# Optimization experiments

Hardware: AMD Instinct MI355X
Metric: run time of the kernel (lower is better)

The kernel has to match this reference:

```python
import jax, jax.numpy as jnp
import numpy as np

N = 50000
D_IN = 128
D_OUT = 128
EPS = 1e-5


def setup_inputs() -> dict:
    key = jax.random.key(0)
    ks = jax.random.split(key, 10)
    x = jax.random.normal(ks[0], (N, D_IN), dtype=jnp.float32)
    edge_index = jax.random.randint(ks[1], (2, 800000), 0, N, dtype=jnp.int64)
    s_in = 1.0 / np.sqrt(D_IN)
    s_out = 1.0 / np.sqrt(D_OUT)
    return {
        "x": x,
        "edge_index": edge_index,
        # SAGEConv 1: lin_l (on aggregated neighbors, with bias), lin_r (root, no bias)
        "w1_l": jax.random.uniform(ks[2], (D_OUT, D_IN), jnp.float32, -s_in, s_in),
        "b1_l": jnp.zeros((D_OUT,), jnp.float32),
        "w1_r": jax.random.uniform(ks[3], (D_OUT, D_IN), jnp.float32, -s_in, s_in),
        # SAGEConv 2
        "w2_l": jax.random.uniform(ks[4], (D_OUT, D_OUT), jnp.float32, -s_out, s_out),
        "b2_l": jnp.zeros((D_OUT,), jnp.float32),
        "w2_r": jax.random.uniform(ks[5], (D_OUT, D_OUT), jnp.float32, -s_out, s_out),
        # BatchNorm affine params
        "bn_gamma": jnp.ones((D_OUT,), jnp.float32),
        "bn_beta": jnp.zeros((D_OUT,), jnp.float32),
    }


def _sage_conv(x, src, dst, w_l, b_l, w_r):
    # mean aggregation of source-node features into target nodes
    msg = x[src]                                              # [E, D]
    agg = jax.ops.segment_sum(msg, dst, num_segments=N)       # [N, D]
    cnt = jax.ops.segment_sum(jnp.ones((src.shape[0],), x.dtype), dst, num_segments=N)
    mean = agg / jnp.maximum(cnt, 1.0)[:, None]
    return mean @ w_l.T + b_l + x @ w_r.T


def _batch_norm(x, gamma, beta):
    mu = jnp.mean(x, axis=0)
    var = jnp.mean(jnp.square(x - mu), axis=0)  # biased, as in torch BN training
    return (x - mu) * jax.lax.rsqrt(var + EPS) * gamma + beta


def reference(x, edge_index, w1_l, b1_l, w1_r, w2_l, b2_l, w2_r, bn_gamma, bn_beta):
    src, dst = edge_index[0], edge_index[1]
    h = _sage_conv(x, src, dst, w1_l, b1_l, w1_r)
    h = _batch_norm(h, bn_gamma, bn_beta)
    h = jax.nn.relu(h)
    out = _sage_conv(h, src, dst, w2_l, b2_l, w2_r)
    return out
```

## Files before the change

### kernel.cpp

```cpp
#include <hip/hip_runtime.h>

#define D 128
#define EPS 1e-5f
#define FB_EPB 8

typedef unsigned int uint;
typedef __attribute__((ext_vector_type(4))) float f32x4;
typedef __attribute__((ext_vector_type(8))) short s16x8;

__device__ __forceinline__ uint pack_bf16(float a, float b)
{
    uint ua = __float_as_uint(a);
    uint ub = __float_as_uint(b);
    ua += 0x7FFFu + ((ua >> 16) & 1u);
    ub += 0x7FFFu + ((ub >> 16) & 1u);
    return (ua >> 16) | (ub & 0xFFFF0000u);
}
__device__ __forceinline__ float bf_lo(uint v) { return __uint_as_float(v << 16); }
__device__ __forceinline__ float bf_hi(uint v) { return __uint_as_float(v & 0xFFFF0000u); }

__global__ void prep_kernel(const float* __restrict__ x, uint* __restrict__ xb, int ncvt,
                            const float* __restrict__ w1l, const float* __restrict__ w1r,
                            const float* __restrict__ w2l, const float* __restrict__ w2r,
                            uint* __restrict__ wb1, uint* __restrict__ wb2)
{
    int idx = blockIdx.x * 256 + threadIdx.x;
    if (idx < ncvt) {
        float4 v = ((const float4*)x)[idx];
        uint2 o;
        o.x = pack_bf16(v.x, v.y);
        o.y = pack_bf16(v.z, v.w);
        ((uint2*)xb)[idx] = o;
    } else if (idx < ncvt + 8192) {
        int r = idx - ncvt;
        int layer = r >> 12;
        int rem = r & 4095;
        int lane = rem & 63;
        int knt = rem >> 6;
        int kstep = knt >> 3, nt = knt & 7;
        int nn = nt * 16 + (lane & 15);
        int kbase = kstep * 32 + (lane >> 4) * 8;
        const float* wl = layer ? w2l : w1l;
        const float* wr = layer ? w2r : w1r;
        uint* wb = layer ? wb2 : wb1;
        float v[8];
#pragma unroll
        for (int j = 0; j < 8; j++) {
            int k = kbase + j;
            v[j] = (k < D) ? wl[nn * D + k] : wr[nn * D + (k - D)];
        }
        uint4 o;
        o.x = pack_bf16(v[0], v[1]);
        o.y = pack_bf16(v[2], v[3]);
        o.z = pack_bf16(v[4], v[5]);
        o.w = pack_bf16(v[6], v[7]);
        ((uint4*)wb)[(kstep * 8 + nt) * 64 + lane] = o;
    } else if (idx < ncvt + 8192 + 32) {
        ((uint2*)xb)[ncvt + (idx - ncvt - 8192)] = make_uint2(0, 0);
    }
}

__global__ __launch_bounds__(512) void bcount_kernel(const int* __restrict__ dst,
                                                     int* __restrict__ bcnt,
                                                     int E, int nblk, int nbuck)
{
    __shared__ int cnt[128];
    int t = threadIdx.x;
    if (t < 128) cnt[t] = 0;
    __syncthreads();
    int e0 = blockIdx.x * (512 * FB_EPB);
#pragma unroll
    for (int k = 0; k < FB_EPB; k++) {
        int e = e0 + k * 512 + t;
        if (e < E) atomicAdd(&cnt[dst[e] >> 9], 1);
    }
    __syncthreads();
    if (t < nbuck) bcnt[t * nblk + blockIdx.x] = cnt[t];
}

__global__ __launch_bounds__(1024) void bscan_kernel(int* __restrict__ bcnt, int M)
{
    __shared__ int sums[1024];
    int t = threadIdx.x;
    int chunk = (M + 1023) / 1024;
    int b0 = t * chunk;
    int b1 = min(b0 + chunk, M);
    int v[32];
    int s = 0;
    for (int i = b0; i < b1; i++) { v[i - b0] = bcnt[i]; s += v[i - b0]; }
    sums[t] = s;
    __syncthreads();
    for (int off = 1; off < 1024; off <<= 1) {
        int u = (t >= off) ? sums[t - off] : 0;
        __syncthreads();
        sums[t] += u;
        __syncthreads();
    }
    int run = sums[t] - s;
    for (int i = b0; i < b1; i++) { bcnt[i] = run; run += v[i - b0]; }
    if (t == 1023) bcnt[M] = sums[1023];
}

__global__ __launch_bounds__(512) void bscatter_kernel(const int* __restrict__ src,
                                                       const int* __restrict__ dst,
                                                       const int* __restrict__ bcnt,
                                                       uint2* __restrict__ ebuf,
                                                       int E, int nblk, int nbuck)
{
    __shared__ int cnt[128], base[128];
    int t = threadIdx.x;
    if (t < 128) cnt[t] = 0;
    __syncthreads();
    int e0 = blockIdx.x * (512 * FB_EPB);
    int s[FB_EPB], d[FB_EPB], loc[FB_EPB];
#pragma unroll
    for (int k = 0; k < FB_EPB; k++) {
        int e = e0 + k * 512 + t;
        if (e < E) {
            s[k] = src[e];
            d[k] = dst[e];
            loc[k] = atomicAdd(&cnt[d[k] >> 9], 1);
        }
    }
    __syncthreads();
    if (t < nbuck) base[t] = bcnt[t * nblk + blockIdx.x];
    __syncthreads();
#pragma unroll
    for (int k = 0; k < FB_EPB; k++) {
        int e = e0 + k * 512 + t;
        if (e < E) {
            int b = d[k] >> 9;
            ebuf[base[b] + loc[k]] = make_uint2((uint)s[k], (uint)d[k]);
        }
    }
}

__global__ __launch_bounds__(512) void pbuild_kernel(const int* __restrict__ bcnt,
                                                     const uint2* __restrict__ ebuf,
                                                     int* __restrict__ rowptr,
                                                     int* __restrict__ col,
                                                     int n, int nblk, int nbuck, int M, int E)
{
    __shared__ int lcnt[512], lscan[512];
    int t = threadIdx.x;
    int b = blockIdx.x;
    int nb = b << 9;
    int e0 = bcnt[b * nblk];
    int e1 = (b + 1 < nbuck) ? bcnt[(b + 1) * nblk] : bcnt[M];
    lcnt[t] = 0;
    __syncthreads();
    for (int i = e0 + t; i < e1; i += 512)
        atomicAdd(&lcnt[(int)ebuf[i].y - nb], 1);
    __syncthreads();
    int s = lcnt[t];
    lscan[t] = s;
    __syncthreads();
    for (int off = 1; off < 512; off <<= 1) {
        int u = (t >= off) ? lscan[t - off] : 0;
        __syncthreads();
        lscan[t] += u;
        __syncthreads();
    }
    int start = e0 + lscan[t] - s;
    int ncnt = min(512, n - nb);
    if (t < ncnt) rowptr[nb + t] = start;
    if (b == nbuck - 1 && t == 0) rowptr[n] = E;
    lscan[t] = start;
    __syncthreads();
    for (int i = e0 + t; i < e1; i += 512) {
        uint2 ed = ebuf[i];
        int p = atomicAdd(&lscan[(int)ed.y - nb], 1);
        col[p] = (int)ed.x;
    }
}

__global__ __launch_bounds__(256) void agg_kernel(const int* __restrict__ rowptr,
                                                  const int* __restrict__ col,
                                                  const uint* __restrict__ featb,
                                                  uint* __restrict__ aggb, int n)
{
    int node = blockIdx.x * 4 + (threadIdx.x >> 6);
    if (node >= n) return;
    int lane = threadIdx.x & 63;
    int sub = lane >> 4, l16 = lane & 15;
    int r0 = rowptr[node], r1 = rowptr[node + 1];
    uint4* out4 = (uint4*)aggb;
    if (r0 == r1) {
        if (lane < 16) out4[(size_t)node * 16 + l16] = make_uint4(0, 0, 0, 0);
        return;
    }
    float acc[8] = {0.f, 0.f, 0.f, 0.f, 0.f, 0.f, 0.f, 0.f};
    const uint4* fb = (const uint4*)featb;
    int last = r1 - 1;

    for (int i = r0; i < r1; i += 16) {
        uint4 v[4];
#pragma unroll
        for (int r = 0; r < 4; r++) {
            int idx = i + r * 4 + sub;
            int cl = col[min(idx, last)];
            int c = (idx < r1) ? cl : n;
            v[r] = fb[(size_t)c * 16 + l16];
        }
#pragma unroll
        for (int r = 0; r < 4; r++) {
            uint4 u = v[r];
            acc[0] += bf_lo(u.x); acc[1] += bf_hi(u.x);
            acc[2] += bf_lo(u.y); acc[3] += bf_hi(u.y);
            acc[4] += bf_lo(u.z); acc[5] += bf_hi(u.z);
            acc[6] += bf_lo(u.w); acc[7] += bf_hi(u.w);
        }
    }
#pragma unroll
    for (int j = 0; j < 8; j++) {
        acc[j] += __shfl_down(acc[j], 32);
        acc[j] += __shfl_down(acc[j], 16);
    }
    if (lane < 16) {
        float inv = 1.0f / (float)(r1 - r0);
        uint4 o;
        o.x = pack_bf16(acc[0] * inv, acc[1] * inv);
        o.y = pack_bf16(acc[2] * inv, acc[3] * inv);
        o.z = pack_bf16(acc[4] * inv, acc[5] * inv);
        o.w = pack_bf16(acc[6] * inv, acc[7] * inv);
        out4[(size_t)node * 16 + l16] = o;
    }
}

#define TSTRIDE 132
template<bool FUSE1>
__global__ __launch_bounds__(256) void conv_kernel(
    const uint* __restrict__ p1b, const uint* __restrict__ p2b,
    const uint* __restrict__ wb, const float* __restrict__ bias,
    float* __restrict__ outf, uint* __restrict__ outb,
    float* __restrict__ pstats, int n)
{
    extern __shared__ float smem[];
    float* tile = smem;
    int w = threadIdx.x >> 6, lane = threadIdx.x & 63;
    int quad = lane >> 4, l15 = lane & 15;
    int nb = blockIdx.x * 64;

    const uint4* p1 = (const uint4*)p1b;
    const uint4* p2 = (const uint4*)p2b;
    const uint4* wv = (const uint4*)wb;

    uint4 B[8][2];
    int nt0 = w * 2;
#pragma unroll
    for (int ks = 0; ks < 8; ks++) {
#pragma unroll
        for (int t = 0; t < 2; t++)
            B[ks][t] = wv[(ks * 8 + nt0 + t) * 64 + lane];
    }

    float bv0 = bias[nt0 * 16 + l15];
    float bv1 = bias[nt0 * 16 + 16 + l15];

    for (int rt = 0; rt < 4; rt++) {
        int node = nb + rt * 16 + l15;
        int nc = min(node, n - 1);
        uint4 A[8];
#pragma unroll
        for (int ks = 0; ks < 4; ks++) A[ks] = p1[(size_t)nc * 16 + ks * 4 + quad];
#pragma unroll
        for (int ks = 0; ks < 4; ks++) A[ks + 4] = p2[(size_t)nc * 16 + ks * 4 + quad];

        f32x4 acc0 = {bv0, bv0, bv0, bv0};
        f32x4 acc1 = {bv1, bv1, bv1, bv1};
#pragma unroll
        for (int ks = 0; ks < 8; ks++) {
            s16x8 a = *(s16x8*)&A[ks];
            acc0 = __builtin_amdgcn_mfma_f32_16x16x32_bf16(a, *(s16x8*)&B[ks][0], acc0, 0, 0, 0);
            acc1 = __builtin_amdgcn_mfma_f32_16x16x32_bf16(a, *(s16x8*)&B[ks][1], acc1, 0, 0, 0);
        }
        int row0 = nb + rt * 16 + quad * 4;
        int colbase = nt0 * 16 + l15;
        if (FUSE1) {
            int rloc0 = rt * 16 + quad * 4;
#pragma unroll
            for (int reg = 0; reg < 4; reg++) {
                bool ok = (row0 + reg) < n;
                tile[(rloc0 + reg) * TSTRIDE + colbase]      = ok ? acc0[reg] : 0.f;
                tile[(rloc0 + reg) * TSTRIDE + colbase + 16] = ok ? acc1[reg] : 0.f;
            }
        } else {
#pragma unroll
            for (int reg = 0; reg < 4; reg++) {
                int row = row0 + reg;
                if (row < n) {
                    outf[(size_t)row * D + colbase] = acc0[reg];
                    outf[(size_t)row * D + colbase + 16] = acc1[reg];
                }
            }
        }
    }

    if (FUSE1) {
        __syncthreads();
        int colj = threadIdx.x & 127, half = threadIdx.x >> 7;
        float s = 0.f, ss = 0.f;
        for (int r = half * 32; r < half * 32 + 32; r++) {
            float v = tile[r * TSTRIDE + colj];
            s += v;
            ss += v * v;
        }
        float* pb = pstats + (size_t)blockIdx.x * 512 + half * 256;
        pb[colj] = s;
        pb[128 + colj] = ss;
        uint4* ob4 = (uint4*)outb;
#pragma unroll
        for (int q4 = 0; q4 < 4; q4++) {
            int idx = q4 * 256 + threadIdx.x;
            int r = idx >> 4, q = idx & 15;
            int row = nb + r;
            if (row < n) {
                float* tr = &tile[r * TSTRIDE + q * 8];
                uint4 o;
                o.x = pack_bf16(tr[0], tr[1]);
                o.y = pack_bf16(tr[2], tr[3]);
                o.z = pack_bf16(tr[4], tr[5]);
                o.w = pack_bf16(tr[6], tr[7]);
                ob4[(size_t)row * 16 + q] = o;
            }
        }
    }
}

__global__ __launch_bounds__(256) void reduce_kernel(const float* __restrict__ pstats,
                                                     float* __restrict__ stats, int nparts)
{
    int j = threadIdx.x;
    int chunk = (nparts + gridDim.x - 1) / gridDim.x;
    int p0 = blockIdx.x * chunk;
    int p1 = min(p0 + chunk, nparts);
    float s = 0.f;
    for (int p = p0; p < p1; p++) s += pstats[(size_t)p * 256 + j];
    unsafeAtomicAdd(&stats[j], s);
}

__global__ void bnfin_kernel(const float* __restrict__ stats, const float* __restrict__ gamma,
                             const float* __restrict__ beta, float* __restrict__ scsh, float n_inv)
{
    int j = threadIdx.x;
    float mean = stats[j] * n_inv;
    float var = fmaxf(stats[128 + j] * n_inv - mean * mean, 0.f);
    float sc = gamma[j] * rsqrtf(var + EPS);
    scsh[j] = sc;
    scsh[128 + j] = beta[j] - mean * sc;
}

__global__ __launch_bounds__(256) void bnapply_kernel(const uint* __restrict__ hb,
                                                      const float* __restrict__ scsh,
                                                      uint* __restrict__ hbn, int total2)
{
    __shared__ float scs[256];
    scs[threadIdx.x] = scsh[threadIdx.x];
    __syncthreads();
    int idx = blockIdx.x * 256 + threadIdx.x;
    if (blockIdx.x == 0 && threadIdx.x < 32)
        ((uint2*)hbn)[total2 + threadIdx.x] = make_uint2(0, 0);
    if (idx >= total2) return;
    int j4 = (idx & 31) * 4;
    uint2 u = ((const uint2*)hb)[idx];
    float e0 = fmaxf(bf_lo(u.x) * scs[j4 + 0] + scs[128 + j4 + 0], 0.f);
    float e1 = fmaxf(bf_hi(u.x) * scs[j4 + 1] + scs[128 + j4 + 1], 0.f);
    float e2 = fmaxf(bf_lo(u.y) * scs[j4 + 2] + scs[128 + j4 + 2], 0.f);
    float e3 = fmaxf(bf_hi(u.y) * scs[j4 + 3] + scs[128 + j4 + 3], 0.f);
    uint2 o;
    o.x = pack_bf16(e0, e1);
    o.y = pack_bf16(e2, e3);
    ((uint2*)hbn)[idx] = o;
}

extern "C" void kernel_launch(void* const* d_in, const int* in_sizes, int n_in,
                              void* d_out, int out_size, void* d_ws, size_t ws_size,
                              hipStream_t stream)
{
    const float* x     = (const float*)d_in[0];
    const int*   ei    = (const int*)d_in[1];
    const float* w1_l  = (const float*)d_in[2];
    const float* b1_l  = (const float*)d_in[3];
    const float* w1_r  = (const float*)d_in[4];
    const float* w2_l  = (const float*)d_in[5];
    const float* b2_l  = (const float*)d_in[6];
    const float* w2_r  = (const float*)d_in[7];
    const float* gamma = (const float*)d_in[8];
    const float* beta  = (const float*)d_in[9];

    int N = in_sizes[0] / D;
    int E = in_sizes[1] / 2;
    const int* src = ei;
    const int* dst = ei + E;

    int cblocks = (N + 63) / 64;
    int nbuck   = (N + 511) >> 9;
    int nblk    = (E + 4095) / 4096;
    int M       = nbuck * nblk;

    uint*  aggb   = (uint*)d_ws;
    uint*  xb     = aggb + (size_t)N * 64;
    uint*  hb     = xb + (size_t)(N + 1) * 64;
    uint*  hbn    = hb + (size_t)N * 64;
    uint*  wb1    = hbn + (size_t)(N + 1) * 64;
    uint*  wb2    = wb1 + 16384;
    uint2* ebuf   = (uint2*)(wb2 + 16384);
    float* stats  = (float*)(ebuf + E);
    float* scsh   = stats + 256;
    float* pstats = scsh + 256;
    int*   rowptr = (int*)(pstats + (size_t)cblocks * 512);
    int*   col    = rowptr + N + 1;
    int*   bcnt   = col + E;

    hipMemsetAsync(stats, 0, 256 * sizeof(float), stream);

    int ncvt = N * 32;
    int pblocks = (ncvt + 8192 + 32 + 255) / 256;
    prep_kernel<<<pblocks, 256, 0, stream>>>(x, xb, ncvt, w1_l, w1_r, w2_l, w2_r, wb1, wb2);

    int ablocks = (N + 3) / 4;

    bcount_kernel<<<nblk, 512, 0, stream>>>(dst, bcnt, E, nblk, nbuck);
    bscan_kernel<<<1, 1024, 0, stream>>>(bcnt, M);
    bscatter_kernel<<<nblk, 512, 0, stream>>>(src, dst, bcnt, ebuf, E, nblk, nbuck);
    pbuild_kernel<<<nbuck, 512, 0, stream>>>(bcnt, ebuf, rowptr, col, N, nblk, nbuck, M, E);

    agg_kernel<<<ablocks, 256, 0, stream>>>(rowptr, col, xb, aggb, N);
    conv_kernel<true><<<cblocks, 256, 64 * TSTRIDE * 4, stream>>>(
        aggb, xb, wb1, b1_l, nullptr, hb, pstats, N);

    reduce_kernel<<<32, 256, 0, stream>>>(pstats, stats, cblocks * 2);
    bnfin_kernel<<<1, 128, 0, stream>>>(stats, gamma, beta, scsh, 1.0f / (float)N);
    bnapply_kernel<<<(N * 32 + 255) / 256, 256, 0, stream>>>(hb, scsh, hbn, N * 32);

    agg_kernel<<<ablocks, 256, 0, stream>>>(rowptr, col, hbn, aggb, N);
    conv_kernel<false><<<cblocks, 256, 1024, stream>>>(
        aggb, hbn, wb2, b2_l, (float*)d_out, nullptr, nullptr, N);
}
```

Measured before the change: 252.0 us.

## Fuse whole GraphSAGE pipeline into one persistent kernel with grid barriers

Replaces the chain of about a dozen kernel launches with one persistent mega-kernel. Its phases (bf16 conversion, CSR build, aggregation, conv, BN stats, BN apply, second layer) are separated by a hierarchical atomic grid barrier. CSR construction moves from bucketed sort to degree count, scan and atomic-cursor scatter. The conv1 epilogue writes bf16 and accumulates BN stats directly, dropping the LDS tile. This removes launch and inter-kernel gaps, but limits occupancy to co-resident blocks, adds barrier spin costs, and makes the col order nondeterministic.

```diff
diff --git a/kernel.cpp b/kernel.cpp
--- a/kernel.cpp
+++ b/kernel.cpp
@@ -2,7 +2,6 @@
 
 #define D 128
 #define EPS 1e-5f
-#define FB_EPB 8
 
 typedef unsigned int uint;
 typedef __attribute__((ext_vector_type(4))) float f32x4;
@@ -19,228 +18,106 @@
 __device__ __forceinline__ float bf_lo(uint v) { return __uint_as_float(v << 16); }
 __device__ __forceinline__ float bf_hi(uint v) { return __uint_as_float(v & 0xFFFF0000u); }
 
-__global__ void prep_kernel(const float* __restrict__ x, uint* __restrict__ xb, int ncvt,
-                            const float* __restrict__ w1l, const float* __restrict__ w1r,
-                            const float* __restrict__ w2l, const float* __restrict__ w2r,
-                            uint* __restrict__ wb1, uint* __restrict__ wb2)
-{
-    int idx = blockIdx.x * 256 + threadIdx.x;
-    if (idx < ncvt) {
-        float4 v = ((const float4*)x)[idx];
-        uint2 o;
-        o.x = pack_bf16(v.x, v.y);
-        o.y = pack_bf16(v.z, v.w);
-        ((uint2*)xb)[idx] = o;
-    } else if (idx < ncvt + 8192) {
-        int r = idx - ncvt;
-        int layer = r >> 12;
-        int rem = r & 4095;
-        int lane = rem & 63;
-        int knt = rem >> 6;
-        int kstep = knt >> 3, nt = knt & 7;
-        int nn = nt * 16 + (lane & 15);
-        int kbase = kstep * 32 + (lane >> 4) * 8;
-        const float* wl = layer ? w2l : w1l;
-        const float* wr = layer ? w2r : w1r;
-        uint* wb = layer ? wb2 : wb1;
-        float v[8];
+struct MP {
+    const float *x, *w1l, *b1l, *w1r, *w2l, *b2l, *w2r, *gamma, *beta;
+    const int *src, *dst;
+    float *outf;
+    uint *xb, *aggb, *hb, *hbn, *wb1, *wb2;
+    int *rowptr, *cursor, *col, *bsum, *bar;
+    float *pstats, *stats, *scsh;
+    int n, e;
+};
+
+__device__ __forceinline__ void grid_barrier(int* bar, int G, int phase)
+{
+    __syncthreads();
+    if (threadIdx.x == 0) {
+        __threadfence();
+        int g = blockIdx.x >> 4;
+        int ngroups = (G + 15) >> 4;
+        int members = min(16, G - (g << 4));
+        int a = __hip_atomic_fetch_add(&bar[g * 32], 1, __ATOMIC_ACQ_REL,
+                                       __HIP_MEMORY_SCOPE_AGENT);
+        if (a + 1 == phase * members)
+            __hip_atomic_fetch_add(&bar[4096], 1, __ATOMIC_ACQ_REL,
+                                   __HIP_MEMORY_SCOPE_AGENT);
+        while (__hip_atomic_load(&bar[4096], __ATOMIC_ACQUIRE,
+                                 __HIP_MEMORY_SCOPE_AGENT) < phase * ngroups)
+            __builtin_amdgcn_s_sleep(2);
+        __threadfence();
+    }
+    __syncthreads();
+}
+
+__device__ __forceinline__ void agg_phase(const int* __restrict__ rowptr,
+                                          const int* __restrict__ col,
+                                          const uint* __restrict__ featb,
+                                          uint* __restrict__ aggb, int n, int G)
+{
+    int tid = threadIdx.x;
+    int wid = tid >> 6, lane = tid & 63;
+    int sub = lane >> 4, l16 = lane & 15;
+    const uint4* fb = (const uint4*)featb;
+    uint4* out4 = (uint4*)aggb;
+    int nlb = (n + 3) >> 2;
+    for (int lb = blockIdx.x; lb < nlb; lb += G) {
+        int node = lb * 4 + wid;
+        if (node >= n) continue;
+        int r0 = rowptr[node], r1 = rowptr[node + 1];
+        if (r0 == r1) {
+            if (lane < 16) out4[(size_t)node * 16 + l16] = make_uint4(0, 0, 0, 0);
+            continue;
+        }
+        float acc[8] = {0.f, 0.f, 0.f, 0.f, 0.f, 0.f, 0.f, 0.f};
+        int last = r1 - 1;
+        for (int i = r0; i < r1; i += 16) {
+            uint4 v[4];
+#pragma unroll
+            for (int r = 0; r < 4; r++) {
+                int idx = i + r * 4 + sub;
+                int cl = col[min(idx, last)];
+                int c = (idx < r1) ? cl : n;
+                v[r] = fb[(size_t)c * 16 + l16];
+            }
+#pragma unroll
+            for (int r = 0; r < 4; r++) {
+                uint4 u = v[r];
+                acc[0] += bf_lo(u.x); acc[1] += bf_hi(u.x);
+                acc[2] += bf_lo(u.y); acc[3] += bf_hi(u.y);
+                acc[4] += bf_lo(u.z); acc[5] += bf_hi(u.z);
+                acc[6] += bf_lo(u.w); acc[7] += bf_hi(u.w);
+            }
+        }
 #pragma unroll
         for (int j = 0; j < 8; j++) {
-            int k = kbase + j;
-            v[j] = (k < D) ? wl[nn * D + k] : wr[nn * D + (k - D)];
-        }
-        uint4 o;
-        o.x = pack_bf16(v[0], v[1]);
-        o.y = pack_bf16(v[2], v[3]);
-        o.z = pack_bf16(v[4], v[5]);
-        o.w = pack_bf16(v[6], v[7]);
-        ((uint4*)wb)[(kstep * 8 + nt) * 64 + lane] = o;
-    } else if (idx < ncvt + 8192 + 32) {
-        ((uint2*)xb)[ncvt + (idx - ncvt - 8192)] = make_uint2(0, 0);
-    }
-}
-
-__global__ __launch_bounds__(512) void bcount_kernel(const int* __restrict__ dst,
-                                                     int* __restrict__ bcnt,
-                                                     int E, int nblk, int nbuck)
-{
-    __shared__ int cnt[128];
-    int t = threadIdx.x;
-    if (t < 128) cnt[t] = 0;
-    __syncthreads();
-    int e0 = blockIdx.x * (512 * FB_EPB);
-#pragma unroll
-    for (int k = 0; k < FB_EPB; k++) {
-        int e = e0 + k * 512 + t;
-        if (e < E) atomicAdd(&cnt[dst[e] >> 9], 1);
-    }
-    __syncthreads();
-    if (t < nbuck) bcnt[t * nblk + blockIdx.x] = cnt[t];
-}
-
-__global__ __launch_bounds__(1024) void bscan_kernel(int* __restrict__ bcnt, int M)
-{
-    __shared__ int sums[1024];
-    int t = threadIdx.x;
-    int chunk = (M + 1023) / 1024;
-    int b0 = t * chunk;
-    int b1 = min(b0 + chunk, M);
-    int v[32];
-    int s = 0;
-    for (int i = b0; i < b1; i++) { v[i - b0] = bcnt[i]; s += v[i - b0]; }
-    sums[t] = s;
-    __syncthreads();
-    for (int off = 1; off < 1024; off <<= 1) {
-        int u = (t >= off) ? sums[t - off] : 0;
-        __syncthreads();
-        sums[t] += u;
-        __syncthreads();
-    }
-    int run = sums[t] - s;
-    for (int i = b0; i < b1; i++) { bcnt[i] = run; run += v[i - b0]; }
-    if (t == 1023) bcnt[M] = sums[1023];
-}
-
-__global__ __launch_bounds__(512) void bscatter_kernel(const int* __restrict__ src,
-                                                       const int* __restrict__ dst,
-                                                       const int* __restrict__ bcnt,
-                                                       uint2* __restrict__ ebuf,
-                                                       int E, int nblk, int nbuck)
-{
-    __shared__ int cnt[128], base[128];
-    int t = threadIdx.x;
-    if (t < 128) cnt[t] = 0;
-    __syncthreads();
-    int e0 = blockIdx.x * (512 * FB_EPB);
-    int s[FB_EPB], d[FB_EPB], loc[FB_EPB];
-#pragma unroll
-    for (int k = 0; k < FB_EPB; k++) {
-        int e = e0 + k * 512 + t;
-        if (e < E) {
-            s[k] = src[e];
-            d[k] = dst[e];
-            loc[k] = atomicAdd(&cnt[d[k] >> 9], 1);
-        }
-    }
-    __syncthreads();
-    if (t < nbuck) base[t] = bcnt[t * nblk + blockIdx.x];
-    __syncthreads();
-#pragma unroll
-    for (int k = 0; k < FB_EPB; k++) {
-        int e = e0 + k * 512 + t;
-        if (e < E) {
-            int b = d[k] >> 9;
-            ebuf[base[b] + loc[k]] = make_uint2((uint)s[k], (uint)d[k]);
-        }
-    }
-}
-
-__global__ __launch_bounds__(512) void pbuild_kernel(const int* __restrict__ bcnt,
-                                                     const uint2* __restrict__ ebuf,
-                                                     int* __restrict__ rowptr,
-                                                     int* __restrict__ col,
-                                                     int n, int nblk, int nbuck, int M, int E)
-{
-    __shared__ int lcnt[512], lscan[512];
-    int t = threadIdx.x;
-    int b = blockIdx.x;
-    int nb = b << 9;
-    int e0 = bcnt[b * nblk];
-    int e1 = (b + 1 < nbuck) ? bcnt[(b + 1) * nblk] : bcnt[M];
-    lcnt[t] = 0;
-    __syncthreads();
-    for (int i = e0 + t; i < e1; i += 512)
-        atomicAdd(&lcnt[(int)ebuf[i].y - nb], 1);
-    __syncthreads();
-    int s = lcnt[t];
-    lscan[t] = s;
-    __syncthreads();
-    for (int off = 1; off < 512; off <<= 1) {
-        int u = (t >= off) ? lscan[t - off] : 0;
-        __syncthreads();
-        lscan[t] += u;
-        __syncthreads();
-    }
-    int start = e0 + lscan[t] - s;
-    int ncnt = min(512, n - nb);
-    if (t < ncnt) rowptr[nb + t] = start;
-    if (b == nbuck - 1 && t == 0) rowptr[n] = E;
-    lscan[t] = start;
-    __syncthreads();
-    for (int i = e0 + t; i < e1; i += 512) {
-        uint2 ed = ebuf[i];
-        int p = atomicAdd(&lscan[(int)ed.y - nb], 1);
-        col[p] = (int)ed.x;
-    }
-}
-
-__global__ __launch_bounds__(256) void agg_kernel(const int* __restrict__ rowptr,
-                                                  const int* __restrict__ col,
-                                                  const uint* __restrict__ featb,
-                                                  uint* __restrict__ aggb, int n)
-{
-    int node = blockIdx.x * 4 + (threadIdx.x >> 6);
-    if (node >= n) return;
-    int lane = threadIdx.x & 63;
-    int sub = lane >> 4, l16 = lane & 15;
-    int r0 = rowptr[node], r1 = rowptr[node + 1];
-    uint4* out4 = (uint4*)aggb;
-    if (r0 == r1) {
-        if (lane < 16) out4[(size_t)node * 16 + l16] = make_uint4(0, 0, 0, 0);
-        return;
-    }
-    float acc[8] = {0.f, 0.f, 0.f, 0.f, 0.f, 0.f, 0.f, 0.f};
-    const uint4* fb = (const uint4*)featb;
-    int last = r1 - 1;
-
-    for (int i = r0; i < r1; i += 16) {
-        uint4 v[4];
-#pragma unroll
-        for (int r = 0; r < 4; r++) {
-            int idx = i + r * 4 + sub;
-            int cl = col[min(idx, last)];
-            int c = (idx < r1) ? cl : n;
-            v[r] = fb[(size_t)c * 16 + l16];
-        }
-#pragma unroll
-        for (int r = 0; r < 4; r++) {
-            uint4 u = v[r];
-            acc[0] += bf_lo(u.x); acc[1] += bf_hi(u.x);
-            acc[2] += bf_lo(u.y); acc[3] += bf_hi(u.y);
-            acc[4] += bf_lo(u.z); acc[5] += bf_hi(u.z);
-            acc[6] += bf_lo(u.w); acc[7] += bf_hi(u.w);
-        }
-    }
-#pragma unroll
-    for (int j = 0; j < 8; j++) {
-        acc[j] += __shfl_down(acc[j], 32);
-        acc[j] += __shfl_down(acc[j], 16);
-    }
-    if (lane < 16) {
-        float inv = 1.0f / (float)(r1 - r0);
-        uint4 o;
-        o.x = pack_bf16(acc[0] * inv, acc[1] * inv);
-        o.y = pack_bf16(acc[2] * inv, acc[3] * inv);
-        o.z = pack_bf16(acc[4] * inv, acc[5] * inv);
-        o.w = pack_bf16(acc[6] * inv, acc[7] * inv);
-        out4[(size_t)node * 16 + l16] = o;
-    }
-}
-
-#define TSTRIDE 132
+            acc[j] += __shfl_down(acc[j], 32);
+            acc[j] += __shfl_down(acc[j], 16);
+        }
+        if (lane < 16) {
+            float inv = 1.0f / (float)(r1 - r0);
+            uint4 o;
+            o.x = pack_bf16(acc[0] * inv, acc[1] * inv);
+            o.y = pack_bf16(acc[2] * inv, acc[3] * inv);
+            o.z = pack_bf16(acc[4] * inv, acc[5] * inv);
+            o.w = pack_bf16(acc[6] * inv, acc[7] * inv);
+            out4[(size_t)node * 16 + l16] = o;
+        }
+    }
+}
+
 template<bool FUSE1>
-__global__ __launch_bounds__(256) void conv_kernel(
-    const uint* __restrict__ p1b, const uint* __restrict__ p2b,
-    const uint* __restrict__ wb, const float* __restrict__ bias,
-    float* __restrict__ outf, uint* __restrict__ outb,
-    float* __restrict__ pstats, int n)
-{
-    extern __shared__ float smem[];
-    float* tile = smem;
-    int w = threadIdx.x >> 6, lane = threadIdx.x & 63;
+__device__ __forceinline__ void conv_phase(const uint* __restrict__ p1b,
+                                           const uint* __restrict__ p2b,
+                                           const uint* __restrict__ wb,
+                                           const float* __restrict__ bias,
+                                           float* __restrict__ outf,
+                                           uint* __restrict__ outb,
+                                           float* __restrict__ pstats,
+                                           int n, int G)
+{
+    int tid = threadIdx.x;
+    int w = tid >> 6, lane = tid & 63;
     int quad = lane >> 4, l15 = lane & 15;
-    int nb = blockIdx.x * 64;
-
     const uint4* p1 = (const uint4*)p1b;
     const uint4* p2 = (const uint4*)p2b;
     const uint4* wv = (const uint4*)wb;
@@ -253,124 +130,226 @@
         for (int t = 0; t < 2; t++)
             B[ks][t] = wv[(ks * 8 + nt0 + t) * 64 + lane];
     }
-
     float bv0 = bias[nt0 * 16 + l15];
     float bv1 = bias[nt0 * 16 + 16 + l15];
 
-    for (int rt = 0; rt < 4; rt++) {
-        int node = nb + rt * 16 + l15;
-        int nc = min(node, n - 1);
-        uint4 A[8];
-#pragma unroll
-        for (int ks = 0; ks < 4; ks++) A[ks] = p1[(size_t)nc * 16 + ks * 4 + quad];
-#pragma unroll
-        for (int ks = 0; ks < 4; ks++) A[ks + 4] = p2[(size_t)nc * 16 + ks * 4 + quad];
-
-        f32x4 acc0 = {bv0, bv0, bv0, bv0};
-        f32x4 acc1 = {bv1, bv1, bv1, bv1};
-#pragma unroll
-        for (int ks = 0; ks < 8; ks++) {
-            s16x8 a = *(s16x8*)&A[ks];
-            acc0 = __builtin_amdgcn_mfma_f32_16x16x32_bf16(a, *(s16x8*)&B[ks][0], acc0, 0, 0, 0);
-            acc1 = __builtin_amdgcn_mfma_f32_16x16x32_bf16(a, *(s16x8*)&B[ks][1], acc1, 0, 0, 0);
-        }
-        int row0 = nb + rt * 16 + quad * 4;
-        int colbase = nt0 * 16 + l15;
-        if (FUSE1) {
-            int rloc0 = rt * 16 + quad * 4;
-#pragma unroll
-            for (int reg = 0; reg < 4; reg++) {
-                bool ok = (row0 + reg) < n;
-                tile[(rloc0 + reg) * TSTRIDE + colbase]      = ok ? acc0[reg] : 0.f;
-                tile[(rloc0 + reg) * TSTRIDE + colbase + 16] = ok ? acc1[reg] : 0.f;
-            }
-        } else {
+    float s0 = 0.f, ss0 = 0.f, s1 = 0.f, ss1 = 0.f;
+    int ncb = (n + 63) >> 6;
+    for (int cb = blockIdx.x; cb < ncb; cb += G) {
+        int nb = cb * 64;
+        for (int rt = 0; rt < 4; rt++) {
+            int node = nb + rt * 16 + l15;
+            int nc = min(node, n - 1);
+            uint4 A[8];
+#pragma unroll
+            for (int ks = 0; ks < 4; ks++) A[ks] = p1[(size_t)nc * 16 + ks * 4 + quad];
+#pragma unroll
+            for (int ks = 0; ks < 4; ks++) A[ks + 4] = p2[(size_t)nc * 16 + ks * 4 + quad];
+
+            f32x4 acc0 = {bv0, bv0, bv0, bv0};
+            f32x4 acc1 = {bv1, bv1, bv1, bv1};
+#pragma unroll
+            for (int ks = 0; ks < 8; ks++) {
+                s16x8 a = *(s16x8*)&A[ks];
+                acc0 = __builtin_amdgcn_mfma_f32_16x16x32_bf16(a, *(s16x8*)&B[ks][0], acc0, 0, 0, 0);
+                acc1 = __builtin_amdgcn_mfma_f32_16x16x32_bf16(a, *(s16x8*)&B[ks][1], acc1, 0, 0, 0);
+            }
+            int row0 = nb + rt * 16 + quad * 4;
+            int colbase = nt0 * 16 + l15;
 #pragma unroll
             for (int reg = 0; reg < 4; reg++) {
                 int row = row0 + reg;
-                if (row < n) {
-                    outf[(size_t)row * D + colbase] = acc0[reg];
-                    outf[(size_t)row * D + colbase + 16] = acc1[reg];
+                bool ok = row < n;
+                if (FUSE1) {
+                    float v0 = ok ? acc0[reg] : 0.f;
+                    float v1 = ok ? acc1[reg] : 0.f;
+                    s0 += v0; ss0 += v0 * v0;
+                    s1 += v1; ss1 += v1 * v1;
+                    float w0 = __shfl_xor(v0, 1);
+                    float w1 = __shfl_xor(v1, 1);
+                    if (!(l15 & 1) && ok) {
+                        uint* orow = outb + (size_t)row * 64 + nt0 * 8 + (l15 >> 1);
+                        orow[0] = pack_bf16(v0, w0);
+                        orow[8] = pack_bf16(v1, w1);
+                    }
+                } else {
+                    if (ok) {
+                        outf[(size_t)row * D + colbase] = acc0[reg];
+                        outf[(size_t)row * D + colbase + 16] = acc1[reg];
+                    }
                 }
             }
         }
     }
-
     if (FUSE1) {
+        s0 += __shfl_down(s0, 32);  s0 += __shfl_down(s0, 16);
+        ss0 += __shfl_down(ss0, 32); ss0 += __shfl_down(ss0, 16);
+        s1 += __shfl_down(s1, 32);  s1 += __shfl_down(s1, 16);
+        ss1 += __shfl_down(ss1, 32); ss1 += __shfl_down(ss1, 16);
+        if (lane < 16) {
+            float* pb = pstats + (size_t)blockIdx.x * 256;
+            int c0 = nt0 * 16 + l15;
+            pb[c0] = s0;       pb[128 + c0] = ss0;
+            pb[c0 + 16] = s1;  pb[128 + c0 + 16] = ss1;
+        }
+    }
+}
+
+__global__ __launch_bounds__(256, 4) void mega_kernel(MP p)
+{
+    __shared__ int ism[256];
+    __shared__ float scs[256];
+    int G = gridDim.x, bid = blockIdx.x, tid = threadIdx.x;
+    int n = p.n, e = p.e;
+    int ph = 0;
+
+    {
+        int ncvt = n * 32;
+        int total0 = ncvt + 8192 + 32;
+        for (int idx = bid * 256 + tid; idx < total0; idx += G * 256) {
+            if (idx < ncvt) {
+                float4 v = ((const float4*)p.x)[idx];
+                uint2 o;
+                o.x = pack_bf16(v.x, v.y);
+                o.y = pack_bf16(v.z, v.w);
+                ((uint2*)p.xb)[idx] = o;
+            } else if (idx < ncvt + 8192) {
+                int r = idx - ncvt;
+                int layer = r >> 12;
+                int rem = r & 4095;
+                int lane = rem & 63;
+                int knt = rem >> 6;
+                int kstep = knt >> 3, nt = knt & 7;
+                int nn = nt * 16 + (lane & 15);
+                int kbase = kstep * 32 + (lane >> 4) * 8;
+                const float* wl = layer ? p.w2l : p.w1l;
+                const float* wr = layer ? p.w2r : p.w1r;
+                uint* wbp = layer ? p.wb2 : p.wb1;
+                float v[8];
+#pragma unroll
+                for (int j = 0; j < 8; j++) {
+                    int k = kbase + j;
+                    v[j] = (k < D) ? wl[nn * D + k] : wr[nn * D + (k - D)];
+                }
+                uint4 o;
+                o.x = pack_bf16(v[0], v[1]);
+                o.y = pack_bf16(v[2], v[3]);
+                o.z = pack_bf16(v[4], v[5]);
+                o.w = pack_bf16(v[6], v[7]);
+                ((uint4*)wbp)[(kstep * 8 + nt) * 64 + lane] = o;
+            } else {
+                ((uint2*)p.xb)[ncvt + (idx - ncvt - 8192)] = make_uint2(0, 0);
+            }
+        }
+        for (int i = bid * 256 + tid; i < n; i += G * 256) p.cursor[i] = 0;
+        if (bid == 0) p.stats[tid] = 0.f;
+    }
+    grid_barrier(p.bar, G, ++ph);
+
+    for (int i = bid * 256 + tid; i < e; i += G * 256)
+        atomicAdd(&p.cursor[p.dst[i]], 1);
+    grid_barrier(p.bar, G, ++ph);
+
+    {
+        int nsb = (n + 255) >> 8;
+        for (int sb = bid; sb < nsb; sb += G) {
+            int idx = sb * 256 + tid;
+            int v = (idx < n) ? p.cursor[idx] : 0;
+            ism[tid] = v;
+            __syncthreads();
+            for (int off = 1; off < 256; off <<= 1) {
+                int u = (tid >= off) ? ism[tid - off] : 0;
+                __syncthreads();
+                ism[tid] += u;
+                __syncthreads();
+            }
+            if (idx < n) p.rowptr[idx] = ism[tid] - v;
+            if (tid == 255) p.bsum[sb] = ism[255];
+            __syncthreads();
+        }
+    }
+    grid_barrier(p.bar, G, ++ph);
+
+    if (bid == 0) {
+        int nsb = (n + 255) >> 8;
+        int v = (tid < nsb) ? p.bsum[tid] : 0;
+        ism[tid] = v;
         __syncthreads();
-        int colj = threadIdx.x & 127, half = threadIdx.x >> 7;
-        float s = 0.f, ss = 0.f;
-        for (int r = half * 32; r < half * 32 + 32; r++) {
-            float v = tile[r * TSTRIDE + colj];
-            s += v;
-            ss += v * v;
-        }
-        float* pb = pstats + (size_t)blockIdx.x * 512 + half * 256;
-        pb[colj] = s;
-        pb[128 + colj] = ss;
-        uint4* ob4 = (uint4*)outb;
-#pragma unroll
-        for (int q4 = 0; q4 < 4; q4++) {
-            int idx = q4 * 256 + threadIdx.x;
-            int r = idx >> 4, q = idx & 15;
-            int row = nb + r;
-            if (row < n) {
-                float* tr = &tile[r * TSTRIDE + q * 8];
-                uint4 o;
-                o.x = pack_bf16(tr[0], tr[1]);
-                o.y = pack_bf16(tr[2], tr[3]);
-                o.z = pack_bf16(tr[4], tr[5]);
-                o.w = pack_bf16(tr[6], tr[7]);
-                ob4[(size_t)row * 16 + q] = o;
-            }
-        }
-    }
-}
-
-__global__ __launch_bounds__(256) void reduce_kernel(const float* __restrict__ pstats,
-                                                     float* __restrict__ stats, int nparts)
-{
-    int j = threadIdx.x;
-    int chunk = (nparts + gridDim.x - 1) / gridDim.x;
-    int p0 = blockIdx.x * chunk;
-    int p1 = min(p0 + chunk, nparts);
-    float s = 0.f;
-    for (int p = p0; p < p1; p++) s += pstats[(size_t)p * 256 + j];
-    unsafeAtomicAdd(&stats[j], s);
-}
-
-__global__ void bnfin_kernel(const float* __restrict__ stats, const float* __restrict__ gamma,
-                             const float* __restrict__ beta, float* __restrict__ scsh, float n_inv)
-{
-    int j = threadIdx.x;
-    float mean = stats[j] * n_inv;
-    float var = fmaxf(stats[128 + j] * n_inv - mean * mean, 0.f);
-    float sc = gamma[j] * rsqrtf(var + EPS);
-    scsh[j] = sc;
-    scsh[128 + j] = beta[j] - mean * sc;
-}
-
-__global__ __launch_bounds__(256) void bnapply_kernel(const uint* __restrict__ hb,
-                                                      const float* __restrict__ scsh,
-                                                      uint* __restrict__ hbn, int total2)
-{
-    __shared__ float scs[256];
-    scs[threadIdx.x] = scsh[threadIdx.x];
-    __syncthreads();
-    int idx = blockIdx.x * 256 + threadIdx.x;
-    if (blockIdx.x == 0 && threadIdx.x < 32)
-        ((uint2*)hbn)[total2 + threadIdx.x] = make_uint2(0, 0);
-    if (idx >= total2) return;
-    int j4 = (idx & 31) * 4;
-    uint2 u = ((const uint2*)hb)[idx];
-    float e0 = fmaxf(bf_lo(u.x) * scs[j4 + 0] + scs[128 + j4 + 0], 0.f);
-    float e1 = fmaxf(bf_hi(u.x) * scs[j4 + 1] + scs[128 + j4 + 1], 0.f);
-    float e2 = fmaxf(bf_lo(u.y) * scs[j4 + 2] + scs[128 + j4 + 2], 0.f);
-    float e3 = fmaxf(bf_hi(u.y) * scs[j4 + 3] + scs[128 + j4 + 3], 0.f);
-    uint2 o;
-    o.x = pack_bf16(e0, e1);
-    o.y = pack_bf16(e2, e3);
-    ((uint2*)hbn)[idx] = o;
+        for (int off = 1; off < 256; off <<= 1) {
+            int u = (tid >= off) ? ism[tid - off] : 0;
+            __syncthreads();
+            ism[tid] += u;
+            __syncthreads();
+        }
+        if (tid < nsb) p.bsum[tid] = ism[tid] - v;
+        if (tid == 0) p.rowptr[n] = e;
+    }
+    grid_barrier(p.bar, G, ++ph);
+
+    for (int i = bid * 256 + tid; i < n; i += G * 256) {
+        int r = p.rowptr[i] + p.bsum[i >> 8];
+        p.rowptr[i] = r;
+        p.cursor[i] = r;
+    }
+    grid_barrier(p.bar, G, ++ph);
+
+    for (int i = bid * 256 + tid; i < e; i += G * 256) {
+        int pp = atomicAdd(&p.cursor[p.dst[i]], 1);
+        p.col[pp] = p.src[i];
+    }
+    grid_barrier(p.bar, G, ++ph);
+
+    agg_phase(p.rowptr, p.col, p.xb, p.aggb, n, G);
+    grid_barrier(p.bar, G, ++ph);
+
+    conv_phase<true>(p.aggb, p.xb, p.wb1, p.b1l, nullptr, p.hb, p.pstats, n, G);
+    grid_barrier(p.bar, G, ++ph);
+
+    if (bid < 32) {
+        int nparts = G;
+        int chunk = (nparts + 31) >> 5;
+        int q0 = bid * chunk, q1 = min(q0 + chunk, nparts);
+        float s = 0.f;
+        for (int q = q0; q < q1; q++) s += p.pstats[(size_t)q * 256 + tid];
+        unsafeAtomicAdd(&p.stats[tid], s);
+    }
+    grid_barrier(p.bar, G, ++ph);
+
+    if (bid == 0 && tid < 128) {
+        float n_inv = 1.0f / (float)n;
+        float mean = p.stats[tid] * n_inv;
+        float var = fmaxf(p.stats[128 + tid] * n_inv - mean * mean, 0.f);
+        float sc = p.gamma[tid] * rsqrtf(var + EPS);
+        p.scsh[tid] = sc;
+        p.scsh[128 + tid] = p.beta[tid] - mean * sc;
+    }
+    grid_barrier(p.bar, G, ++ph);
+
+    {
+        scs[tid] = p.scsh[tid];
+        __syncthreads();
+        int total2 = n * 32;
+        for (int idx = bid * 256 + tid; idx < total2; idx += G * 256) {
+            int j4 = (idx & 31) * 4;
+            uint2 u = ((const uint2*)p.hb)[idx];
+            float e0 = fmaxf(bf_lo(u.x) * scs[j4 + 0] + scs[128 + j4 + 0], 0.f);
+            float e1 = fmaxf(bf_hi(u.x) * scs[j4 + 1] + scs[128 + j4 + 1], 0.f);
+            float e2 = fmaxf(bf_lo(u.y) * scs[j4 + 2] + scs[128 + j4 + 2], 0.f);
+            float e3 = fmaxf(bf_hi(u.y) * scs[j4 + 3] + scs[128 + j4 + 3], 0.f);
+            uint2 o;
+            o.x = pack_bf16(e0, e1);
+            o.y = pack_bf16(e2, e3);
+            ((uint2*)p.hbn)[idx] = o;
+        }
+        if (bid == 0 && tid < 32)
+            ((uint2*)p.hbn)[total2 + tid] = make_uint2(0, 0);
+    }
+    grid_barrier(p.bar, G, ++ph);
+
+    agg_phase(p.rowptr, p.col, p.hbn, p.aggb, n, G);
+    grid_barrier(p.bar, G, ++ph);
+
+    conv_phase<false>(p.aggb, p.hbn, p.wb2, p.b2l, p.outf, nullptr, nullptr, n, G);
 }
 
 extern "C" void kernel_launch(void* const* d_in, const int* in_sizes, int n_in,
@@ -390,13 +369,6 @@
 
     int N = in_sizes[0] / D;
     int E = in_sizes[1] / 2;
-    const int* src = ei;
-    const int* dst = ei + E;
-
-    int cblocks = (N + 63) / 64;
-    int nbuck   = (N + 511) >> 9;
-    int nblk    = (E + 4095) / 4096;
-    int M       = nbuck * nblk;
 
     uint*  aggb   = (uint*)d_ws;
     uint*  xb     = aggb + (size_t)N * 64;
@@ -404,36 +376,46 @@
     uint*  hbn    = hb + (size_t)N * 64;
     uint*  wb1    = hbn + (size_t)(N + 1) * 64;
     uint*  wb2    = wb1 + 16384;
-    uint2* ebuf   = (uint2*)(wb2 + 16384);
-    float* stats  = (float*)(ebuf + E);
+    float* pstats = (float*)(wb2 + 16384);
+    float* stats  = pstats + (size_t)2048 * 256;
     float* scsh   = stats + 256;
-    float* pstats = scsh + 256;
-    int*   rowptr = (int*)(pstats + (size_t)cblocks * 512);
-    int*   col    = rowptr + N + 1;
-    int*   bcnt   = col + E;
-
-    hipMemsetAsync(stats, 0, 256 * sizeof(float), stream);
-
-    int ncvt = N * 32;
-    int pblocks = (ncvt + 8192 + 32 + 255) / 256;
-    prep_kernel<<<pblocks, 256, 0, stream>>>(x, xb, ncvt, w1_l, w1_r, w2_l, w2_r, wb1, wb2);
-
-    int ablocks = (N + 3) / 4;
-
-    bcount_kernel<<<nblk, 512, 0, stream>>>(dst, bcnt, E, nblk, nbuck);
-    bscan_kernel<<<1, 1024, 0, stream>>>(bcnt, M);
-    bscatter_kernel<<<nblk, 512, 0, stream>>>(src, dst, bcnt, ebuf, E, nblk, nbuck);
-    pbuild_kernel<<<nbuck, 512, 0, stream>>>(bcnt, ebuf, rowptr, col, N, nblk, nbuck, M, E);
-
-    agg_kernel<<<ablocks, 256, 0, stream>>>(rowptr, col, xb, aggb, N);
-    conv_kernel<true><<<cblocks, 256, 64 * TSTRIDE * 4, stream>>>(
-        aggb, xb, wb1, b1_l, nullptr, hb, pstats, N);
-
-    reduce_kernel<<<32, 256, 0, stream>>>(pstats, stats, cblocks * 2);
-    bnfin_kernel<<<1, 128, 0, stream>>>(stats, gamma, beta, scsh, 1.0f / (float)N);
-    bnapply_kernel<<<(N * 32 + 255) / 256, 256, 0, stream>>>(hb, scsh, hbn, N * 32);
-
-    agg_kernel<<<ablocks, 256, 0, stream>>>(rowptr, col, hbn, aggb, N);
-    conv_kernel<false><<<cblocks, 256, 1024, stream>>>(
-        aggb, hbn, wb2, b2_l, (float*)d_out, nullptr, nullptr, N);
-}
+    int*   rowptr = (int*)(scsh + 256);
+    int*   cursor = rowptr + (N + 1);
+    int*   col    = cursor + N;
+    int*   bsum   = col + E;
+    int*   bar    = bsum + 256;
+
+    static int g_blocks = 0;
+    if (g_blocks == 0) {
+        int mb = 0;
+        if (hipOccupancyMaxActiveBlocksPerMultiprocessor(&mb, mega_kernel, 256, 0)
+                != hipSuccess || mb < 1)
+            mb = 1;
+        if (mb > 8) mb = 8;
+        int cu = 256;
+        int dev = 0;
+        hipDeviceProp_t prop;
+        if (hipGetDevice(&dev) == hipSuccess &&
+            hipGetDeviceProperties(&prop, dev) == hipSuccess &&
+            prop.multiProcessorCount > 0)
+            cu = prop.multiProcessorCount;
+        g_blocks = mb * cu;
+        if (g_blocks > 2048) g_blocks = 2048;
+        if (g_blocks < 64) g_blocks = 64;
+    }
+
+    hipMemsetAsync(bar, 0, 4104 * sizeof(int), stream);
+
+    MP p;
+    p.x = x; p.w1l = w1_l; p.b1l = b1_l; p.w1r = w1_r;
+    p.w2l = w2_l; p.b2l = b2_l; p.w2r = w2_r;
+    p.gamma = gamma; p.beta = beta;
+    p.src = ei; p.dst = ei + E;
+    p.outf = (float*)d_out;
+    p.xb = xb; p.aggb = aggb; p.hb = hb; p.hbn = hbn; p.wb1 = wb1; p.wb2 = wb2;
+    p.rowptr = rowptr; p.cursor = cursor; p.col = col; p.bsum = bsum; p.bar = bar;
+    p.pstats = pstats; p.stats = stats; p.scsh = scsh;
+    p.n = N; p.e = E;
+
+    mega_kernel<<<g_blocks, 256, 0, stream>>>(p);
+}
```

Result: slower. 990.9 us (+293.1%).
